# Performance work log

Measured on AMD Instinct MI355X. Metric: run time of the kernel, lower is better.

Reference implementation:

```python
import jax, jax.numpy as jnp
import numpy as np

B, S, DIN, DOUT = 2, 2048, 4096, 4096


def setup_inputs() -> dict:
    key = jax.random.key(0)
    k1, k2 = jax.random.split(key)
    x = jax.random.normal(k1, (B, S, DIN), dtype=jnp.float32)
    weight = jax.random.normal(k2, (DOUT, DIN), dtype=jnp.float32) * 0.02
    # xnor init for row scaling pattern
    mean = weight.mean(-1, keepdims=True)                      # [DOUT,1]
    scale = jnp.abs(weight - mean).mean(-1, keepdims=True)     # [DOUT,1]
    wscale = scale
    wbias = mean
    return {"x": x, "weight": weight, "wscale": wscale, "wbias": wbias}


def reference(x, weight, wscale, wbias):
    # STE binarization: forward = sign(weight) (grad handled in bwd module)
    w_bin = jnp.sign(weight)
    w = wscale * w_bin + wbias                                 # [DOUT, DIN]
    # F.linear(x, w): x @ w.T, no bias
    out = jnp.einsum('bsk,nk->bsn', x, w)
    return out
```

## Files before the change

kernel.cpp:

```cpp
#include <hip/hip_runtime.h>
#include <stdint.h>


#define MDIM 4096
#define NDIM 4096
#define KDIM 4096

typedef int int4v __attribute__((ext_vector_type(4)));

__device__ __forceinline__ int pack4_rn(float a, float b, float c, float d, float inv) {
  int ia = __float2int_rn(a * inv) & 0xff;
  int ib = __float2int_rn(b * inv) & 0xff;
  int ic = __float2int_rn(c * inv) & 0xff;
  int id = __float2int_rn(d * inv) & 0xff;
  return ia | (ib << 8) | (ic << 16) | (id << 24);
}

__device__ __forceinline__ int sgn8(float v) {
  return (v > 0.f) ? 1 : ((v < 0.f) ? 0xff : 0);
}

__global__ __launch_bounds__(256) void prep_kernel(
    const float* __restrict__ x, const float* __restrict__ w,
    char* __restrict__ xq, char* __restrict__ wsg,
    float* __restrict__ xscale, float* __restrict__ sumx) {
  const int b = blockIdx.x;
  const int tid = threadIdx.x;
  if (b < MDIM) {
    const int row = b;
    const float4* xr = (const float4*)(x + (size_t)row * KDIM);
    float4 v[4];
    float s = 0.f, amax = 0.f;
#pragma unroll
    for (int u = 0; u < 4; ++u) {
      v[u] = xr[u * 256 + tid];
      s += v[u].x + v[u].y + v[u].z + v[u].w;
      amax = fmaxf(amax, fmaxf(fmaxf(fabsf(v[u].x), fabsf(v[u].y)),
                               fmaxf(fabsf(v[u].z), fabsf(v[u].w))));
    }
#pragma unroll
    for (int off = 32; off > 0; off >>= 1) {
      s += __shfl_down(s, off, 64);
      amax = fmaxf(amax, __shfl_down(amax, off, 64));
    }
    __shared__ float rs[4], rm[4], bcast;
    if ((tid & 63) == 0) { rs[tid >> 6] = s; rm[tid >> 6] = amax; }
    __syncthreads();
    if (tid == 0) {
      sumx[row] = rs[0] + rs[1] + rs[2] + rs[3];
      float mt = fmaxf(fmaxf(rm[0], rm[1]), fmaxf(rm[2], rm[3]));
      xscale[row] = mt * (1.f / 127.f);
      bcast = (mt > 0.f) ? 127.f / mt : 0.f;
    }
    __syncthreads();
    const float inv = bcast;
    int* xo = (int*)(xq + (size_t)row * KDIM);
#pragma unroll
    for (int u = 0; u < 4; ++u)
      xo[u * 256 + tid] = pack4_rn(v[u].x, v[u].y, v[u].z, v[u].w, inv);
  } else {
    const size_t base = (size_t)(b - MDIM) * (256 * 4);
    const float4* wr = (const float4*)w;
    int* wo = (int*)wsg;
#pragma unroll
    for (int u = 0; u < 4; ++u) {
      size_t i = base + u * 256 + tid;
      float4 v = wr[i];
      wo[i] = sgn8(v.x) | (sgn8(v.y) << 8) | (sgn8(v.z) << 16) | (sgn8(v.w) << 24);
    }
  }
}

__global__ __launch_bounds__(256) void gemm_bin_i8_kernel(
    const char* __restrict__ A, const char* __restrict__ Bs,
    const float* __restrict__ wscale, const float* __restrict__ wbias,
    const float* __restrict__ xscale, const float* __restrict__ sumx,
    float* __restrict__ C) {
  __shared__ __align__(16) char sA0[128 * 64], sA1[128 * 64];
  __shared__ __align__(16) char sB0[128 * 64], sB1[128 * 64];

  const int bn = blockIdx.x & 31;
  const int bm = blockIdx.x >> 5;
  const int tm0 = bm * 128, tn0 = bn * 128;
  const int tid = threadIdx.x;
  const int lane = tid & 63, wave = tid >> 6;
  const int quad = lane >> 4, l16 = lane & 15;
  const int wmo = (wave >> 1) * 64, wno = (wave & 1) * 64;

  int4v acc[4][4];
  const int4v zero4 = {0, 0, 0, 0};
#pragma unroll
  for (int i = 0; i < 4; ++i)
#pragma unroll
    for (int j = 0; j < 4; ++j) acc[i][j] = zero4;

  int st_row[2], st_lblk[2];
#pragma unroll
  for (int q = 0; q < 2; ++q) {
    int u = q * 256 + tid;
    st_row[q] = u >> 2;
    st_lblk[q] = (u & 3) ^ ((st_row[q] >> 1) & 3);
  }
  const char* gA0 = A  + (size_t)(tm0 + st_row[0]) * KDIM + st_lblk[0] * 16;
  const char* gA1 = A  + (size_t)(tm0 + st_row[1]) * KDIM + st_lblk[1] * 16;
  const char* gB0 = Bs + (size_t)(tn0 + st_row[0]) * KDIM + st_lblk[0] * 16;
  const char* gB1 = Bs + (size_t)(tn0 + st_row[1]) * KDIM + st_lblk[1] * 16;
  const int ld0 = tid * 16, ld1 = 4096 + tid * 16;

  int aOff[4], bOff[4];
#pragma unroll
  for (int i = 0; i < 4; ++i) {
    int r = wmo + i * 16 + l16;
    aOff[i] = r * 64 + (quad ^ ((r >> 1) & 3)) * 16;
  }
#pragma unroll
  for (int j = 0; j < 4; ++j) {
    int r = wno + j * 16 + l16;
    bOff[j] = r * 64 + (quad ^ ((r >> 1) & 3)) * 16;
  }

#define STAGE(dstA, dstB, kofs)                                                  \
  do {                                                                           \
    __builtin_amdgcn_global_load_lds(                                            \
        (const __attribute__((address_space(1))) void*)(gA0 + (kofs)),           \
        (__attribute__((address_space(3))) void*)((dstA) + ld0), 16, 0, 0);      \
    __builtin_amdgcn_global_load_lds(                                            \
        (const __attribute__((address_space(1))) void*)(gA1 + (kofs)),           \
        (__attribute__((address_space(3))) void*)((dstA) + ld1), 16, 0, 0);      \
    __builtin_amdgcn_global_load_lds(                                            \
        (const __attribute__((address_space(1))) void*)(gB0 + (kofs)),           \
        (__attribute__((address_space(3))) void*)((dstB) + ld0), 16, 0, 0);      \
    __builtin_amdgcn_global_load_lds(                                            \
        (const __attribute__((address_space(1))) void*)(gB1 + (kofs)),           \
        (__attribute__((address_space(3))) void*)((dstB) + ld1), 16, 0, 0);      \
  } while (0)

#define COMPUTE(srcA, srcB)                                                      \
  do {                                                                           \
    int4v af[4], bfr[4];                                                         \
    _Pragma("unroll") for (int i = 0; i < 4; ++i)                                \
        af[i] = *(const int4v*)((srcA) + aOff[i]);                               \
    _Pragma("unroll") for (int j = 0; j < 4; ++j)                                \
        bfr[j] = *(const int4v*)((srcB) + bOff[j]);                              \
    _Pragma("unroll") for (int i = 0; i < 4; ++i)                                \
        _Pragma("unroll") for (int j = 0; j < 4; ++j)                            \
            acc[i][j] = __builtin_amdgcn_mfma_i32_16x16x64_i8(af[i], bfr[j],     \
                                                              acc[i][j], 0, 0, 0);\
  } while (0)

  STAGE(sA0, sB0, 0);
  for (int kt = 0; kt < KDIM; kt += 128) {
    __syncthreads();
    if (kt + 64 < KDIM) STAGE(sA1, sB1, kt + 64);
    COMPUTE(sA0, sB0);
    __syncthreads();
    if (kt + 128 < KDIM) STAGE(sA0, sB0, kt + 128);
    COMPUTE(sA1, sB1);
  }
#undef STAGE
#undef COMPUTE

  float wsv[4], wbv[4];
#pragma unroll
  for (int j = 0; j < 4; ++j) {
    int n = tn0 + wno + j * 16 + l16;
    wsv[j] = wscale[n];
    wbv[j] = wbias[n];
  }
#pragma unroll
  for (int i = 0; i < 4; ++i) {
#pragma unroll
    for (int r = 0; r < 4; ++r) {
      int m = tm0 + wmo + i * 16 + quad * 4 + r;
      float xs = xscale[m];
      float sx = sumx[m];
      float* crow = C + (size_t)m * NDIM + tn0 + wno + l16;
#pragma unroll
      for (int j = 0; j < 4; ++j) {
        crow[j * 16] = wsv[j] * xs * (float)acc[i][j][r] + wbv[j] * sx;
      }
    }
  }
}

extern "C" void kernel_launch(void* const* d_in, const int* in_sizes, int n_in,
                              void* d_out, int out_size, void* d_ws, size_t ws_size,
                              hipStream_t stream) {
  const float* x      = (const float*)d_in[0];
  const float* weight = (const float*)d_in[1];
  const float* wscale = (const float*)d_in[2];
  const float* wbias  = (const float*)d_in[3];
  float* out = (float*)d_out;

  char* xq  = (char*)d_ws;
  char* wsg = xq + (size_t)MDIM * KDIM;
  float* xscale = (float*)(wsg + (size_t)NDIM * KDIM);
  float* sumx   = xscale + MDIM;

  prep_kernel<<<MDIM + (NDIM * KDIM) / (16 * 256), 256, 0, stream>>>(
      x, weight, xq, wsg, xscale, sumx);
  gemm_bin_i8_kernel<<<(MDIM / 128) * (NDIM / 128), 256, 0, stream>>>(
      xq, wsg, wscale, wbias, xscale, sumx, out);
}
```

Before: 248.1 us.

## Triple-buffer LDS staging with partial vmcnt waits in int8 GEMM

After: 244.6 us. No clear change (-1.4%).

```diff
diff --git a/kernel.cpp b/kernel.cpp
--- a/kernel.cpp
+++ b/kernel.cpp
@@ -76,8 +76,8 @@
     const float* __restrict__ wscale, const float* __restrict__ wbias,
     const float* __restrict__ xscale, const float* __restrict__ sumx,
     float* __restrict__ C) {
-  __shared__ __align__(16) char sA0[128 * 64], sA1[128 * 64];
-  __shared__ __align__(16) char sB0[128 * 64], sB1[128 * 64];
+  __shared__ __align__(16) char sA0[128 * 64], sA1[128 * 64], sA2[128 * 64];
+  __shared__ __align__(16) char sB0[128 * 64], sB1[128 * 64], sB2[128 * 64];
 
   const int bn = blockIdx.x & 31;
   const int bm = blockIdx.x >> 5;
@@ -148,15 +148,32 @@
                                                               acc[i][j], 0, 0, 0);\
   } while (0)
 
+#define SYNC_KEEP4() asm volatile("s_waitcnt vmcnt(4)\n\ts_barrier" ::: "memory")
+#define SYNC_ALL()   asm volatile("s_waitcnt vmcnt(0)\n\ts_barrier" ::: "memory")
+
+#define ITER(cA, cB, pA, pB, kofs_next)                                          \
+  do {                                                                           \
+    SYNC_KEEP4();                                                                \
+    STAGE(pA, pB, (kofs_next));                                                  \
+    COMPUTE(cA, cB);                                                             \
+  } while (0)
+
   STAGE(sA0, sB0, 0);
-  for (int kt = 0; kt < KDIM; kt += 128) {
-    __syncthreads();
-    if (kt + 64 < KDIM) STAGE(sA1, sB1, kt + 64);
-    COMPUTE(sA0, sB0);
-    __syncthreads();
-    if (kt + 128 < KDIM) STAGE(sA0, sB0, kt + 128);
-    COMPUTE(sA1, sB1);
-  }
+  STAGE(sA1, sB1, 64);
+  for (int i = 0; i < 60; i += 3) {
+    ITER(sA0, sB0, sA2, sB2, (i + 2) * 64);
+    ITER(sA1, sB1, sA0, sB0, (i + 3) * 64);
+    ITER(sA2, sB2, sA1, sB1, (i + 4) * 64);
+  }
+  ITER(sA0, sB0, sA2, sB2, 62 * 64);
+  ITER(sA1, sB1, sA0, sB0, 63 * 64);
+  SYNC_KEEP4();
+  COMPUTE(sA2, sB2);
+  SYNC_ALL();
+  COMPUTE(sA0, sB0);
+#undef ITER
+#undef SYNC_KEEP4
+#undef SYNC_ALL
 #undef STAGE
 #undef COMPUTE
 
```
